# Optimization experiments

Hardware: AMD Instinct MI355X
Metric: run time of the kernel (lower is better)

Reference implementation:

```python
import jax, jax.numpy as jnp
import numpy as np

N, E, DIN, DH, H, B, C = 20000, 320000, 128, 64, 8, 16, 10
NEG_SLOPE = 0.2


def segment_softmax(e, dst, num_nodes):
    # e: [E, H] edge scores, softmax over edges sharing the same dst node
    m = jax.ops.segment_max(e, dst, num_segments=num_nodes)          # [N, H]
    ex = jnp.exp(e - m[dst])                                          # [E, H]
    den = jax.ops.segment_sum(ex, dst, num_segments=num_nodes)       # [N, H]
    return ex / den[dst]


def gat_layer(h, edge_src, edge_dst, W, attn_l, attn_r, bias):
    # h: [N, F_in] -> out: [N, H, DH]  (DGL GATConv math)
    feat = (h @ W).reshape(-1, H, DH)                                 # [N, H, DH]
    el = jnp.einsum('nhd,hd->nh', feat, attn_l)                       # [N, H]
    er = jnp.einsum('nhd,hd->nh', feat, attn_r)                       # [N, H]
    e = jax.nn.leaky_relu(el[edge_src] + er[edge_dst], NEG_SLOPE)     # [E, H]
    alpha = segment_softmax(e, edge_dst, feat.shape[0])               # [E, H]
    msg = feat[edge_src] * alpha[..., None]                           # [E, H, DH]
    out = jax.ops.segment_sum(msg, edge_dst, num_segments=feat.shape[0])
    return out + bias[None, :, :]


def setup_inputs() -> dict:
    key = jax.random.key(0)
    ks = jax.random.split(key, 16)
    s_in = 1.0 / np.sqrt(DIN)
    s_h = 1.0 / np.sqrt(DH)
    return {
        'g_feats': jax.random.normal(ks[0], (N, DIN), jnp.float32),
        'edge_src': jax.random.randint(ks[1], (E,), 0, N),
        'edge_dst': jax.random.randint(ks[2], (E,), 0, N),
        'node_graph_ids': jnp.sort(jax.random.randint(ks[3], (N,), 0, B)),
        'W_in': jax.random.normal(ks[4], (DIN, DH), jnp.float32) * s_in,
        'b_in': jnp.zeros((DH,), jnp.float32),
        'W1': jax.random.normal(ks[5], (DH, H * DH), jnp.float32) * s_h,
        'attn_l1': jax.random.normal(ks[6], (H, DH), jnp.float32) * s_h,
        'attn_r1': jax.random.normal(ks[7], (H, DH), jnp.float32) * s_h,
        'bias1': jnp.zeros((H, DH), jnp.float32),
        'W2': jax.random.normal(ks[8], (DH, H * DH), jnp.float32) * s_h,
        'attn_l2': jax.random.normal(ks[9], (H, DH), jnp.float32) * s_h,
        'attn_r2': jax.random.normal(ks[10], (H, DH), jnp.float32) * s_h,
        'bias2': jnp.zeros((H, DH), jnp.float32),
        'W_head': jax.random.normal(ks[11], (DH, C), jnp.float32) * s_h,
        'b_head': jnp.zeros((C,), jnp.float32),
    }


def reference(g_feats, edge_src, edge_dst, node_graph_ids,
              W_in, b_in, W1, attn_l1, attn_r1, bias1,
              W2, attn_l2, attn_r2, bias2, W_head, b_head):
    h = g_feats @ W_in + b_in                                          # input layer
    h = gat_layer(h, edge_src, edge_dst, W1, attn_l1, attn_r1, bias1)  # [N,H,DH]
    h = jax.nn.relu(h.mean(axis=1))                                    # head-mean + relu
    h = gat_layer(h, edge_src, edge_dst, W2, attn_l2, attn_r2, bias2)
    h = h.mean(axis=1)                                                 # [N, DH]
    # mean readout per graph
    sums = jax.ops.segment_sum(h, node_graph_ids, num_segments=B)      # [B, DH]
    cnt = jax.ops.segment_sum(jnp.ones((h.shape[0],), h.dtype), node_graph_ids, num_segments=B)
    hg = sums / jnp.maximum(cnt, 1.0)[:, None]
    return jax.nn.softmax(hg @ W_head + b_head, axis=-1)               # [B, C]
```

## Files before the change

kernel.cpp:

```cpp
#include <hip/hip_runtime.h>
#include <hip/hip_bf16.h>
#include <math.h>


#define NEG_SLOPE 0.2f

typedef float f32x2 __attribute__((ext_vector_type(2)));
typedef float f32x4 __attribute__((ext_vector_type(4)));
typedef short bf16x8 __attribute__((ext_vector_type(8)));

__device__ __forceinline__ float bf2f(__hip_bfloat16 b) { return __bfloat162float(b); }
__device__ __forceinline__ unsigned short f2bfu(float x) {
    __hip_bfloat16 b = __float2bfloat16(x);
    return *(unsigned short*)&b;
}

__device__ __forceinline__ unsigned char f2fp8(float x) {
    unsigned int u = __builtin_amdgcn_cvt_pk_fp8_f32(x, x, 0, false);
    return (unsigned char)(u & 0xff);
}
__device__ __forceinline__ void unpack8_fp8(uint2 u, float* f) {
    f32x2 a = __builtin_amdgcn_cvt_pk_f32_fp8(u.x, false);
    f32x2 b = __builtin_amdgcn_cvt_pk_f32_fp8(u.x, true);
    f32x2 c = __builtin_amdgcn_cvt_pk_f32_fp8(u.y, false);
    f32x2 d = __builtin_amdgcn_cvt_pk_f32_fp8(u.y, true);
    f[0] = a[0]; f[1] = a[1]; f[2] = b[0]; f[3] = b[1];
    f[4] = c[0]; f[5] = c[1]; f[6] = d[0]; f[7] = d[1];
}

__global__ __launch_bounds__(256) void prep_all(const float* __restrict__ W1,
                                                const float* __restrict__ W2,
                                                unsigned short* __restrict__ Bz1,
                                                unsigned short* __restrict__ Bz2,
                                                int* __restrict__ cnt,
                                                float* __restrict__ hg, int N) {
    int b = blockIdx.x;
    if (b < 32) {
        const float* W = (b < 16) ? W1 : W2;
        unsigned short* Wswz = (b < 16) ? Bz1 : Bz2;
        int fid = (b & 15) * 256 + threadIdx.x;
        int lane = fid & 63;
        int ks = (fid >> 6) & 1;
        int ctg = fid >> 7;
        int col = ctg * 16 + (lane & 15);
        int k0 = ks * 32 + ((lane >> 4) << 3);
        unsigned short v[8];
#pragma unroll
        for (int j = 0; j < 8; ++j) v[j] = f2bfu(W[(k0 + j) * 512 + col]);
        ushort4* dst = (ushort4*)(Wswz + (size_t)fid * 8);
        dst[0] = make_ushort4(v[0], v[1], v[2], v[3]);
        dst[1] = make_ushort4(v[4], v[5], v[6], v[7]);
    } else {
        for (int i = (b - 32) * 256 + threadIdx.x; i < N; i += 4 * 256) cnt[i] = 0;
        if (b == 32) {
            for (int i = threadIdx.x; i < 16 * 64; i += 256) hg[i] = 0.f;
        }
    }
}

__global__ void hist_kernel(const int* __restrict__ dst, int* __restrict__ cnt, int E) {
    int e = blockIdx.x * 256 + threadIdx.x;
    if (e < E) atomicAdd(&cnt[dst[e]], 1);
}

__global__ __launch_bounds__(1024) void scan_kernel(const int* __restrict__ cnt,
                                                    int* __restrict__ row_start,
                                                    int* __restrict__ cursor, int N) {
    __shared__ int part[1024];
    int t = threadIdx.x;
    int CH = (N + 1023) >> 10;
    int beg = t * CH;
    int end = beg + CH; if (end > N) end = N;
    if (beg > N) beg = N;
    int local = 0;
    for (int i = beg; i < end; ++i) local += cnt[i];
    part[t] = local;
    __syncthreads();
    for (int off = 1; off < 1024; off <<= 1) {
        int v = (t >= off) ? part[t - off] : 0;
        __syncthreads();
        part[t] += v;
        __syncthreads();
    }
    int run = part[t] - local;
    for (int i = beg; i < end; ++i) {
        row_start[i] = run; cursor[i] = run;
        run += cnt[i];
    }
    if (t == 1023) row_start[N] = run;
}

__global__ void scatter_kernel(const int* __restrict__ src, const int* __restrict__ dst,
                               int* __restrict__ cursor, int* __restrict__ src_sorted, int E) {
    int e = blockIdx.x * 256 + threadIdx.x;
    if (e < E) {
        int p = atomicAdd(&cursor[dst[e]], 1);
        src_sorted[p] = src[e];
    }
}

__global__ __launch_bounds__(256) void in_gemm(const float* __restrict__ g,
                                               const float* __restrict__ W,
                                               const float* __restrict__ b,
                                               float* __restrict__ h0, int N) {
    __shared__ float gt[128][36];
    int t = threadIdx.x;
    int n0 = blockIdx.x * 32;
#pragma unroll
    for (int i = 0; i < 4; ++i) {
        int ch = t + i * 256;
        int r = ch >> 5, k0 = (ch & 31) << 2;
        float4 v = (n0 + r < N) ? *(const float4*)(g + (size_t)(n0 + r) * 128 + k0)
                                : make_float4(0.f, 0.f, 0.f, 0.f);
        gt[k0 + 0][r] = v.x; gt[k0 + 1][r] = v.y; gt[k0 + 2][r] = v.z; gt[k0 + 3][r] = v.w;
    }
    __syncthreads();
    int c = t & 63, rg = t >> 6;
    float acc[8];
#pragma unroll
    for (int j = 0; j < 8; ++j) acc[j] = 0.f;
#pragma unroll 4
    for (int k = 0; k < 128; ++k) {
        float w = W[k * 64 + c];
        const float* hp = &gt[k][rg * 8];
        float4 ha = *(const float4*)hp;
        float4 hb = *(const float4*)(hp + 4);
        acc[0] = fmaf(ha.x, w, acc[0]);
        acc[1] = fmaf(ha.y, w, acc[1]);
        acc[2] = fmaf(ha.z, w, acc[2]);
        acc[3] = fmaf(ha.w, w, acc[3]);
        acc[4] = fmaf(hb.x, w, acc[4]);
        acc[5] = fmaf(hb.y, w, acc[5]);
        acc[6] = fmaf(hb.z, w, acc[6]);
        acc[7] = fmaf(hb.w, w, acc[7]);
    }
    float bb = b[c];
#pragma unroll
    for (int j = 0; j < 8; ++j) {
        int r = rg * 8 + j;
        if (n0 + r < N) h0[(size_t)(n0 + r) * 64 + c] = acc[j] + bb;
    }
}

__global__ __launch_bounds__(512) void feat_gemm(const float* __restrict__ hin,
                                                 const unsigned short* __restrict__ Wswz,
                                                 const float* __restrict__ al,
                                                 const float* __restrict__ ar,
                                                 unsigned char* __restrict__ feat8,
                                                 __hip_bfloat16* __restrict__ el,
                                                 __hip_bfloat16* __restrict__ er, int N) {
    __shared__ unsigned short shA[32][72];
    __shared__ unsigned char sfp8[32][512];
    int t = threadIdx.x;
    int n0 = blockIdx.x * 32;
    {
        int r = t >> 4, c0 = (t & 15) << 2;
        float4 v = (n0 + r < N) ? *(const float4*)(hin + (size_t)(n0 + r) * 64 + c0)
                                : make_float4(0.f, 0.f, 0.f, 0.f);
        *(ushort4*)&shA[r][c0] = make_ushort4(f2bfu(v.x), f2bfu(v.y), f2bfu(v.z), f2bfu(v.w));
    }
    __syncthreads();

    int lane = t & 63;
    int w = t >> 6;
    int lr = lane & 15;
    int lg = lane >> 4;

    bf16x8 afrag[2][2];
#pragma unroll
    for (int rt = 0; rt < 2; ++rt)
#pragma unroll
        for (int ks = 0; ks < 2; ++ks)
            afrag[rt][ks] = *(const bf16x8*)&shA[rt * 16 + lr][ks * 32 + lg * 8];

    bf16x8 bfrag[4][2];
#pragma unroll
    for (int ct = 0; ct < 4; ++ct)
#pragma unroll
        for (int ks = 0; ks < 2; ++ks) {
            int fid = ((w * 4 + ct) * 2 + ks) * 64 + lane;
            bfrag[ct][ks] = *(const bf16x8*)(Wswz + (size_t)fid * 8);
        }

    f32x4 acc[2][4];
#pragma unroll
    for (int rt = 0; rt < 2; ++rt)
#pragma unroll
        for (int ct = 0; ct < 4; ++ct)
            acc[rt][ct] = (f32x4){0.f, 0.f, 0.f, 0.f};

#pragma unroll
    for (int rt = 0; rt < 2; ++rt)
#pragma unroll
        for (int ct = 0; ct < 4; ++ct) {
            acc[rt][ct] = __builtin_amdgcn_mfma_f32_16x16x32_bf16(afrag[rt][0], bfrag[ct][0], acc[rt][ct], 0, 0, 0);
            acc[rt][ct] = __builtin_amdgcn_mfma_f32_16x16x32_bf16(afrag[rt][1], bfrag[ct][1], acc[rt][ct], 0, 0, 0);
        }

#pragma unroll
    for (int rt = 0; rt < 2; ++rt)
#pragma unroll
        for (int ct = 0; ct < 4; ++ct) {
            int col = w * 64 + ct * 16 + lr;
#pragma unroll
            for (int j = 0; j < 4; ++j)
                sfp8[rt * 16 + lg * 4 + j][col] = f2fp8(acc[rt][ct][j]);
        }

    float alv[4], arv[4];
#pragma unroll
    for (int ct = 0; ct < 4; ++ct) {
        alv[ct] = al[w * 64 + ct * 16 + lr];
        arv[ct] = ar[w * 64 + ct * 16 + lr];
    }
    float elp[2][4], erp[2][4];
#pragma unroll
    for (int rt = 0; rt < 2; ++rt)
#pragma unroll
        for (int j = 0; j < 4; ++j) {
            float sl = 0.f, sr = 0.f;
#pragma unroll
            for (int ct = 0; ct < 4; ++ct) {
                sl = fmaf(acc[rt][ct][j], alv[ct], sl);
                sr = fmaf(acc[rt][ct][j], arv[ct], sr);
            }
            elp[rt][j] = sl; erp[rt][j] = sr;
        }
#pragma unroll
    for (int off = 1; off < 16; off <<= 1)
#pragma unroll
        for (int rt = 0; rt < 2; ++rt)
#pragma unroll
            for (int j = 0; j < 4; ++j) {
                elp[rt][j] += __shfl_xor(elp[rt][j], off, 64);
                erp[rt][j] += __shfl_xor(erp[rt][j], off, 64);
            }
    if (lr == 0) {
#pragma unroll
        for (int rt = 0; rt < 2; ++rt)
#pragma unroll
            for (int j = 0; j < 4; ++j) {
                int r = rt * 16 + lg * 4 + j;
                if (n0 + r < N) {
                    el[(size_t)(n0 + r) * 8 + w] = __float2bfloat16(elp[rt][j]);
                    er[(size_t)(n0 + r) * 8 + w] = __float2bfloat16(erp[rt][j]);
                }
            }
    }

    __syncthreads();
    {
        const uint4* src = (const uint4*)&sfp8[0][0];
        uint4* dst = (uint4*)(feat8 + (size_t)n0 * 512);
        int i0 = t * 2;
        if ((size_t)n0 * 512 + (size_t)(i0 + 2) * 16 <= (size_t)N * 512) {
            dst[i0] = src[i0];
            dst[i0 + 1] = src[i0 + 1];
        }
    }
}

template <bool RELU>
__global__ __launch_bounds__(256, 8) void gat_aggregate(
    const unsigned char* __restrict__ feat8, const __hip_bfloat16* __restrict__ el,
    const __hip_bfloat16* __restrict__ er, const float* __restrict__ bias,
    const int* __restrict__ row_start, const int* __restrict__ src_sorted,
    float* __restrict__ hout, int N) {
    int lane = threadIdx.x & 63;
    int n = blockIdx.x * 4 + (threadIdx.x >> 6);
    if (n >= N) return;
    int h = lane >> 3;
    float erh = bf2f(er[(size_t)n * 8 + h]);
    int row = row_start[n];
    int deg = row_start[n + 1] - row;
    const unsigned char* featl = feat8 + lane * 8;

    float acc[8];
#pragma unroll
    for (int j = 0; j < 8; ++j) acc[j] = 0.f;
    float den = 0.f;

    for (int base = 0; base < deg; base += 64) {
        int cnt = min(deg - base, 64);
        int sv = (lane < cnt) ? src_sorted[row + base + lane] : 0;
        int nsub = cnt & ~7;
        for (int i0 = 0; i0 < nsub; i0 += 8) {
            int se = __shfl(sv, i0 + (lane & 7), 64);
            float ve = bf2f(el[(size_t)se * 8 + h]) + erh;
            ve = fmaxf(ve, NEG_SLOPE * ve);
            float am = __expf(ve);
            int hb = lane & 0x38;
#pragma unroll
            for (int e = 0; e < 8; ++e) {
                float a = __shfl(am, hb | e, 64);
                int s = __shfl(sv, i0 + e, 64);
                uint2 u = *(const uint2*)(featl + (size_t)s * 512);
                den += a;
                float f[8];
                unpack8_fp8(u, f);
#pragma unroll
                for (int j = 0; j < 8; ++j) acc[j] = fmaf(a, f[j], acc[j]);
            }
        }
        for (int i = nsub; i < cnt; ++i) {
            int s = __shfl(sv, i, 64);
            uint2 u = *(const uint2*)(featl + (size_t)s * 512);
            float v = bf2f(el[(size_t)s * 8 + h]) + erh;
            v = fmaxf(v, NEG_SLOPE * v);
            float a = __expf(v);
            den += a;
            float f[8];
            unpack8_fp8(u, f);
#pragma unroll
            for (int j = 0; j < 8; ++j) acc[j] = fmaf(a, f[j], acc[j]);
        }
    }

    float invd = deg > 0 ? 1.f / den : 0.f;
    const float4* bp = (const float4*)(bias + lane * 8);
    float4 b0 = bp[0], b1 = bp[1];
    float o[8];
    o[0] = fmaf(acc[0], invd, b0.x); o[1] = fmaf(acc[1], invd, b0.y);
    o[2] = fmaf(acc[2], invd, b0.z); o[3] = fmaf(acc[3], invd, b0.w);
    o[4] = fmaf(acc[4], invd, b1.x); o[5] = fmaf(acc[5], invd, b1.y);
    o[6] = fmaf(acc[6], invd, b1.z); o[7] = fmaf(acc[7], invd, b1.w);

#pragma unroll
    for (int off = 8; off < 64; off <<= 1)
#pragma unroll
        for (int j = 0; j < 8; ++j)
            o[j] += __shfl_xor(o[j], off, 64);

    if (lane < 8) {
#pragma unroll
        for (int j = 0; j < 8; ++j) {
            o[j] *= 0.125f;
            if (RELU) o[j] = fmaxf(o[j], 0.f);
        }
        float4* op = (float4*)(hout + (size_t)n * 64 + lane * 8);
        op[0] = make_float4(o[0], o[1], o[2], o[3]);
        op[1] = make_float4(o[4], o[5], o[6], o[7]);
    }
}

__global__ __launch_bounds__(256) void readout_partial(const float* __restrict__ h2,
                                                       const int* __restrict__ gid,
                                                       float* __restrict__ hg, int N) {
    int c = threadIdx.x & 63;
    int r = threadIdx.x >> 6;
    int n0 = blockIdx.x * 256;
    float sum = 0.f; int cur = -1;
    int nend = n0 + 256; if (nend > N) nend = N;
    for (int n = n0 + r; n < nend; n += 4) {
        int g = gid[n];
        if (g != cur) {
            if (cur >= 0) atomicAdd(&hg[cur * 64 + c], sum);
            cur = g; sum = 0.f;
        }
        sum += h2[(size_t)n * 64 + c];
    }
    if (cur >= 0) atomicAdd(&hg[cur * 64 + c], sum);
}

__global__ __launch_bounds__(256) void head_kernel(const float* __restrict__ hg_sum,
                                                   const int* __restrict__ gid,
                                                   const float* __restrict__ W_head,
                                                   const float* __restrict__ b_head,
                                                   float* __restrict__ out, int N) {
    __shared__ int scnt[16];
    __shared__ float shg[16 * 64];
    __shared__ float slog[16 * 10];
    int t = threadIdx.x;
    if (t < 16) scnt[t] = 0;
    __syncthreads();
    for (int n = t; n < N; n += 256) atomicAdd(&scnt[gid[n]], 1);
    __syncthreads();
    for (int i = t; i < 1024; i += 256) {
        int g = i >> 6;
        shg[i] = hg_sum[i] / fmaxf((float)scnt[g], 1.f);
    }
    __syncthreads();
    if (t < 160) {
        int g = t / 10, c = t % 10;
        float acc = b_head[c];
#pragma unroll 16
        for (int k = 0; k < 64; ++k) acc = fmaf(shg[g * 64 + k], W_head[k * 10 + c], acc);
        slog[g * 10 + c] = acc;
    }
    __syncthreads();
    if (t < 16) {
        float mx = -INFINITY;
#pragma unroll
        for (int c = 0; c < 10; ++c) mx = fmaxf(mx, slog[t * 10 + c]);
        float e[10], s = 0.f;
#pragma unroll
        for (int c = 0; c < 10; ++c) { e[c] = __expf(slog[t * 10 + c] - mx); s += e[c]; }
        float inv = 1.f / s;
#pragma unroll
        for (int c = 0; c < 10; ++c) out[t * 10 + c] = e[c] * inv;
    }
}

extern "C" void kernel_launch(void* const* d_in, const int* in_sizes, int n_in,
                              void* d_out, int out_size, void* d_ws, size_t ws_size,
                              hipStream_t stream) {
    const float* g_feats  = (const float*)d_in[0];
    const int*   edge_src = (const int*)d_in[1];
    const int*   edge_dst = (const int*)d_in[2];
    const int*   gids     = (const int*)d_in[3];
    const float* W_in     = (const float*)d_in[4];
    const float* b_in     = (const float*)d_in[5];
    const float* W1       = (const float*)d_in[6];
    const float* attn_l1  = (const float*)d_in[7];
    const float* attn_r1  = (const float*)d_in[8];
    const float* bias1    = (const float*)d_in[9];
    const float* W2       = (const float*)d_in[10];
    const float* attn_l2  = (const float*)d_in[11];
    const float* attn_r2  = (const float*)d_in[12];
    const float* bias2    = (const float*)d_in[13];
    const float* W_head   = (const float*)d_in[14];
    const float* b_head   = (const float*)d_in[15];
    float* out = (float*)d_out;

    const int N = in_sizes[3];
    const int E = in_sizes[1];

    unsigned char* feat8 = (unsigned char*)d_ws;
    float* h0 = (float*)(feat8 + (size_t)N * 512);
    float* h1 = h0 + (size_t)N * 64;
    float* h2 = h1 + (size_t)N * 64;
    float* hg = h2 + (size_t)N * 64;
    __hip_bfloat16* el = (__hip_bfloat16*)(hg + 16 * 64);
    __hip_bfloat16* er = el + (size_t)N * 8;
    unsigned short* Wz1 = (unsigned short*)(er + (size_t)N * 8);
    unsigned short* Wz2 = Wz1 + 32768;
    int* cnt        = (int*)(Wz2 + 32768);
    int* row_start  = cnt + N;
    int* cursor     = row_start + N + 1;
    int* src_sorted = cursor + N;

    int eb = (E + 255) / 256;
    int nb4 = (N + 3) / 4;
    int nb32 = (N + 31) / 32;
    int nb256 = (N + 255) / 256;

    prep_all<<<36, 256, 0, stream>>>(W1, W2, Wz1, Wz2, cnt, hg, N);
    hist_kernel<<<eb, 256, 0, stream>>>(edge_dst, cnt, E);
    scan_kernel<<<1, 1024, 0, stream>>>(cnt, row_start, cursor, N);
    scatter_kernel<<<eb, 256, 0, stream>>>(edge_src, edge_dst, cursor, src_sorted, E);

    in_gemm<<<nb32, 256, 0, stream>>>(g_feats, W_in, b_in, h0, N);

    feat_gemm<<<nb32, 512, 0, stream>>>(h0, Wz1, attn_l1, attn_r1, feat8, el, er, N);
    gat_aggregate<true><<<nb4, 256, 0, stream>>>(feat8, el, er, bias1, row_start, src_sorted, h1, N);

    feat_gemm<<<nb32, 512, 0, stream>>>(h1, Wz2, attn_l2, attn_r2, feat8, el, er, N);
    gat_aggregate<false><<<nb4, 256, 0, stream>>>(feat8, el, er, bias2, row_start, src_sorted, h2, N);

    readout_partial<<<nb256, 256, 0, stream>>>(h2, gids, hg, N);
    head_kernel<<<1, 256, 0, stream>>>(hg, gids, W_head, b_head, out, N);
}
```

Baseline: 288.8 us.

## Fuse CSR build into GEMM launches and binary-search graph counts

The edge histogram now runs as extra blocks of the input GEMM launch, and the edge scatter runs as extra blocks of the first feature GEMM launch. This removes two kernel launches and lets the independent edge-sorting work overlap with GEMM blocks. The head kernel now gets per-graph node counts by binary search over the sorted graph ids, which relies on them being sorted, instead of running shared-memory atomics over all nodes. The fused launches mix block types that use different amounts of resources, which may affect scheduling.

```diff
diff --git a/kernel.cpp b/kernel.cpp
--- a/kernel.cpp
+++ b/kernel.cpp
@@ -58,11 +58,6 @@
     }
 }
 
-__global__ void hist_kernel(const int* __restrict__ dst, int* __restrict__ cnt, int E) {
-    int e = blockIdx.x * 256 + threadIdx.x;
-    if (e < E) atomicAdd(&cnt[dst[e]], 1);
-}
-
 __global__ __launch_bounds__(1024) void scan_kernel(const int* __restrict__ cnt,
                                                     int* __restrict__ row_start,
                                                     int* __restrict__ cursor, int N) {
@@ -90,21 +85,20 @@
     if (t == 1023) row_start[N] = run;
 }
 
-__global__ void scatter_kernel(const int* __restrict__ src, const int* __restrict__ dst,
-                               int* __restrict__ cursor, int* __restrict__ src_sorted, int E) {
-    int e = blockIdx.x * 256 + threadIdx.x;
-    if (e < E) {
-        int p = atomicAdd(&cursor[dst[e]], 1);
-        src_sorted[p] = src[e];
-    }
-}
-
-__global__ __launch_bounds__(256) void in_gemm(const float* __restrict__ g,
-                                               const float* __restrict__ W,
-                                               const float* __restrict__ b,
-                                               float* __restrict__ h0, int N) {
+__global__ __launch_bounds__(256) void in_gemm_hist(const float* __restrict__ g,
+                                                    const float* __restrict__ W,
+                                                    const float* __restrict__ b,
+                                                    float* __restrict__ h0,
+                                                    const int* __restrict__ edge_dst,
+                                                    int* __restrict__ cnt,
+                                                    int N, int E, int nbGemm) {
     __shared__ float gt[128][36];
     int t = threadIdx.x;
+    if (blockIdx.x >= nbGemm) {
+        int e = (blockIdx.x - nbGemm) * 256 + t;
+        if (e < E) atomicAdd(&cnt[edge_dst[e]], 1);
+        return;
+    }
     int n0 = blockIdx.x * 32;
 #pragma unroll
     for (int i = 0; i < 4; ++i) {
@@ -142,16 +136,30 @@
     }
 }
 
+template <bool FUSE_SCATTER>
 __global__ __launch_bounds__(512) void feat_gemm(const float* __restrict__ hin,
                                                  const unsigned short* __restrict__ Wswz,
                                                  const float* __restrict__ al,
                                                  const float* __restrict__ ar,
                                                  unsigned char* __restrict__ feat8,
                                                  __hip_bfloat16* __restrict__ el,
-                                                 __hip_bfloat16* __restrict__ er, int N) {
+                                                 __hip_bfloat16* __restrict__ er,
+                                                 const int* __restrict__ edge_src,
+                                                 const int* __restrict__ edge_dst,
+                                                 int* __restrict__ cursor,
+                                                 int* __restrict__ src_sorted,
+                                                 int N, int E, int nbGemm) {
     __shared__ unsigned short shA[32][72];
     __shared__ unsigned char sfp8[32][512];
     int t = threadIdx.x;
+    if (FUSE_SCATTER && blockIdx.x >= nbGemm) {
+        int e = (blockIdx.x - nbGemm) * 512 + t;
+        if (e < E) {
+            int p = atomicAdd(&cursor[edge_dst[e]], 1);
+            src_sorted[p] = edge_src[e];
+        }
+        return;
+    }
     int n0 = blockIdx.x * 32;
     {
         int r = t >> 4, c0 = (t & 15) << 2;
@@ -371,9 +379,18 @@
     __shared__ float shg[16 * 64];
     __shared__ float slog[16 * 10];
     int t = threadIdx.x;
-    if (t < 16) scnt[t] = 0;
-    __syncthreads();
-    for (int n = t; n < N; n += 256) atomicAdd(&scnt[gid[n]], 1);
+    if (t < 17) {
+        int lo = 0, hi = N;
+        while (lo < hi) { int m = (lo + hi) >> 1; if (gid[m] < t) lo = m + 1; else hi = m; }
+        if (t < 16) scnt[t] = lo;
+        else shg[0] = 0.f;
+        if (t == 16) slog[0] = (float)lo;
+    }
+    __syncthreads();
+    if (t < 16) {
+        int hi = (t == 15) ? (int)slog[0] : scnt[t + 1];
+        scnt[t] = hi - scnt[t];
+    }
     __syncthreads();
     for (int i = t; i < 1024; i += 256) {
         int g = i >> 6;
@@ -439,22 +456,26 @@
     int* cursor     = row_start + N + 1;
     int* src_sorted = cursor + N;
 
-    int eb = (E + 255) / 256;
     int nb4 = (N + 3) / 4;
     int nb32 = (N + 31) / 32;
     int nb256 = (N + 255) / 256;
+    int eb256 = (E + 255) / 256;
+    int eb512 = (E + 511) / 512;
 
     prep_all<<<36, 256, 0, stream>>>(W1, W2, Wz1, Wz2, cnt, hg, N);
-    hist_kernel<<<eb, 256, 0, stream>>>(edge_dst, cnt, E);
+    in_gemm_hist<<<nb32 + eb256, 256, 0, stream>>>(g_feats, W_in, b_in, h0,
+                                                   edge_dst, cnt, N, E, nb32);
     scan_kernel<<<1, 1024, 0, stream>>>(cnt, row_start, cursor, N);
-    scatter_kernel<<<eb, 256, 0, stream>>>(edge_src, edge_dst, cursor, src_sorted, E);
-
-    in_gemm<<<nb32, 256, 0, stream>>>(g_feats, W_in, b_in, h0, N);
-
-    feat_gemm<<<nb32, 512, 0, stream>>>(h0, Wz1, attn_l1, attn_r1, feat8, el, er, N);
+    feat_gemm<true><<<nb32 + eb512, 512, 0, stream>>>(h0, Wz1, attn_l1, attn_r1,
+                                                      feat8, el, er,
+                                                      edge_src, edge_dst, cursor, src_sorted,
+                                                      N, E, nb32);
     gat_aggregate<true><<<nb4, 256, 0, stream>>>(feat8, el, er, bias1, row_start, src_sorted, h1, N);
 
-    feat_gemm<<<nb32, 512, 0, stream>>>(h1, Wz2, attn_l2, attn_r2, feat8, el, er, N);
+    feat_gemm<false><<<nb32, 512, 0, stream>>>(h1, Wz2, attn_l2, attn_r2,
+                                               feat8, el, er,
+                                               nullptr, nullptr, nullptr, nullptr,
+                                               N, E, nb32);
     gat_aggregate<false><<<nb4, 256, 0, stream>>>(feat8, el, er, bias2, row_start, src_sorted, h2, N);
 
     readout_partial<<<nb256, 256, 0, stream>>>(h2, gids, hg, N);
```

Result: faster. 265.5 us (-8.1%).
